# Kernel optimization log

Measured on AMD Instinct MI355X. Metric: run time of the kernel, lower is better.

Reference implementation:

```python
import jax, jax.numpy as jnp
import numpy as np

BN_EPS = 1e-5


def _binarize_act(x):
    # sign(x) forward, clipped STE backward (grad passes where |x|<1)
    xc = jnp.clip(x, -1.0, 1.0)
    return xc + jax.lax.stop_gradient(jnp.sign(x) - xc)


def _binarize_weight(w):
    # XNOR/ReActNet: per-out-channel scale * sign(w); clipped-STE gradient
    scale = jax.lax.stop_gradient(jnp.mean(jnp.abs(w), axis=(1, 2, 3), keepdims=True))
    wc = jnp.clip(w, -1.0, 1.0)
    return wc + jax.lax.stop_gradient(scale * jnp.sign(w) - wc)


def setup_inputs() -> dict:
    key = jax.random.key(0)
    ks = jax.random.split(key, 8)
    B, C, H, W = 64, 64, 56, 56
    P = 64  # planes == inplanes (stride 1, no downsample)
    x = jax.random.normal(ks[0], (B, C, H, W), dtype=jnp.float32)
    bias0 = jnp.zeros((1, C, 1, 1), dtype=jnp.float32)
    w = jax.random.normal(ks[1], (P, C, 3, 3), dtype=jnp.float32) * 0.1
    gamma = jnp.ones((P,), dtype=jnp.float32)
    beta = jnp.zeros((P,), dtype=jnp.float32)
    run_mean = jax.random.normal(ks[2], (P,), dtype=jnp.float32) * 0.1
    run_var = jax.random.uniform(ks[3], (P,), dtype=jnp.float32, minval=0.5, maxval=1.5)
    bias1 = jnp.zeros((1, P, 1, 1), dtype=jnp.float32)
    alpha = jnp.full((P,), 0.25, dtype=jnp.float32)  # PReLU default init
    bias2 = jnp.zeros((1, P, 1, 1), dtype=jnp.float32)
    return {"x": x, "bias0": bias0, "w": w, "gamma": gamma, "beta": beta,
            "run_mean": run_mean, "run_var": run_var, "bias1": bias1,
            "alpha": alpha, "bias2": bias2}


def reference(x, bias0, w, gamma, beta, run_mean, run_var, bias1, alpha, bias2):
    residual = x
    out = x + bias0                      # move0 (LearnableBias)
    out = _binarize_act(out)             # BinAct: sign, clipped STE
    bw = _binarize_weight(w)             # BinConv weight binarization
    out = jax.lax.conv_general_dilated(
        out, bw, window_strides=(1, 1), padding=((1, 1), (1, 1)),
        dimension_numbers=("NCHW", "OIHW", "NCHW"))
    # BatchNorm2d (inference form with running stats)
    inv = gamma / jnp.sqrt(run_var + BN_EPS)
    out = out * inv[None, :, None, None] + (beta - run_mean * inv)[None, :, None, None]
    out = out + residual                 # residual add (downsample is None)
    out = out + bias1                    # move1
    a = alpha[None, :, None, None]
    out = jnp.where(out >= 0, out, a * out)  # PReLU
    out = out + bias2                    # move2
    return out
```

## Files before the change

kernel.cpp:

```cpp
#include <hip/hip_runtime.h>

typedef unsigned long long u64;
typedef unsigned int u32;

#define BATCH 64
#define CH    64
#define HH    56
#define WW    56
#define HW    3136
#define NBAND 14
#define NBLK  (BATCH * NBAND)

__global__ __launch_bounds__(256)
void fold_kernel(const float* __restrict__ w,
                 const float* __restrict__ gamma,
                 const float* __restrict__ beta,
                 const float* __restrict__ rmean,
                 const float* __restrict__ rvar,
                 const float* __restrict__ bias1,
                 const float* __restrict__ alpha,
                 const float* __restrict__ bias2,
                 u64* __restrict__ wtab,
                 float* __restrict__ kc) {
    __shared__ float red[4];
    const int tid = threadIdx.x;
    const int lane = tid & 63;
    const int wv = tid >> 6;
    const int p = blockIdx.x;
    const float* wp = w + p * 576;

    float s = 0.f;
    for (int i = tid; i < 576; i += 256) s += fabsf(wp[i]);
#pragma unroll
    for (int off = 32; off > 0; off >>= 1) s += __shfl_down(s, off);
    if (lane == 0) red[wv] = s;
    __syncthreads();

    if (wv == 0) {
        u64 m[9];
#pragma unroll
        for (int t = 0; t < 9; ++t) {
            m[t] = __ballot(wp[lane * 9 + t] > 0.f);
            if (lane == 0) wtab[p * 12 + t] = m[t];
        }
        if (lane == 0) {
            float scale = (red[0] + red[1] + red[2] + red[3]) * (1.0f / 576.0f);
            float inv = gamma[p] * rsqrtf(rvar[p] + 1e-5f);
            float am = scale * inv;
            float bd = beta[p] - rmean[p] * inv + bias1[p];
            float pt[9];
#pragma unroll
            for (int t = 0; t < 9; ++t) pt[t] = (float)__popcll(m[t]);
            const float cL = pt[0] + pt[3] + pt[6];
            const float cR = pt[2] + pt[5] + pt[8];
            const float rT = pt[0] + pt[1] + pt[2];
            const float rB = pt[6] + pt[7] + pt[8];
            float Ci[3][3] = {
                {0.f, cL,                 cR},
                {rT,  rT + pt[3] + pt[6], rT + pt[5] + pt[8]},
                {rB,  rB + pt[0] + pt[3], rB + pt[2] + pt[5]}};
            float nv[3][3] = {{9, 6, 6}, {6, 4, 4}, {6, 4, 4}};
#pragma unroll
            for (int wc = 0; wc < 3; ++wc)
#pragma unroll
                for (int lc = 0; lc < 3; ++lc)
                    kc[(wc * 3 + lc) * 64 + p] =
                        fmaf(am, 64.f * nv[wc][lc] + 2.f * Ci[wc][lc], bd);
            float* cf = (float*)(wtab + p * 12 + 9);
            cf[0] = -2.f * am;
            cf[1] = alpha[p];
            cf[2] = bias2[p];
            cf[3] = 0.f;
            wtab[p * 12 + 11] = 0;
        }
    }
}

__global__ __launch_bounds__(512, 6)
void fused_kernel(const float* __restrict__ x,
                  const float* __restrict__ bias0,
                  const u64* __restrict__ wtab,
                  const float* __restrict__ kc,
                  float* __restrict__ out) {
    __shared__ __align__(16) u64 Lsgn[6][58];
    __shared__ __align__(16) float kcsm[576];

    const int tid = threadIdx.x;
    const int lane = tid & 63;
    const int wv = tid >> 6;

    for (int i = tid; i < 576; i += 512) kcsm[i] = kc[i];

    const int bid = blockIdx.x;
    const int wg = (bid & 7) * 112 + (bid >> 3);
    const int b = wg / NBAND;
    const int band = wg - b * NBAND;
    const int r0 = band * 4;

    if (wv < 6) {
        const int ir = r0 - 1 + wv;
        const bool rowok = (unsigned)ir < (unsigned)HH;
        u64 mine = 0;
        if (rowok) {
            const float* xp = x + ((size_t)(b * CH + lane)) * HW + ir * WW;
            const float bz = bias0[lane];
#pragma unroll
            for (int q = 0; q < 14; ++q) {
                float4 v = *(const float4*)(xp + q * 4);
                u64 m0 = __ballot(v.x + bz > 0.f);
                u64 m1 = __ballot(v.y + bz > 0.f);
                u64 m2 = __ballot(v.z + bz > 0.f);
                u64 m3 = __ballot(v.w + bz > 0.f);
                mine = (lane == q * 4 + 0) ? m0 : mine;
                mine = (lane == q * 4 + 1) ? m1 : mine;
                mine = (lane == q * 4 + 2) ? m2 : mine;
                mine = (lane == q * 4 + 3) ? m3 : mine;
            }
        }
        if (lane < WW)        Lsgn[wv][1 + lane] = mine;
        else if (lane == 56)  Lsgn[wv][0] = 0;
        else if (lane == 57)  Lsgn[wv][57] = 0;
    }
    __syncthreads();

    const int rl = wv & 3;
    const int ph = __builtin_amdgcn_readfirstlane((wv >> 2) << 5);
    const int h = r0 + rl;
    const int wl = min(lane, WW - 1);
    const bool active = lane < WW;

    u64 A0 = Lsgn[rl + 0][wl + 0];
    u64 A1 = Lsgn[rl + 0][wl + 1];
    u64 A2 = Lsgn[rl + 0][wl + 2];
    u64 A3 = Lsgn[rl + 1][wl + 0];
    u64 A4 = Lsgn[rl + 1][wl + 1];
    u64 A5 = Lsgn[rl + 1][wl + 2];
    u64 A6 = Lsgn[rl + 2][wl + 0];
    u64 A7 = Lsgn[rl + 2][wl + 1];
    u64 A8 = Lsgn[rl + 2][wl + 2];
    asm volatile("" : "+v"(A0), "+v"(A1), "+v"(A2), "+v"(A3), "+v"(A4),
                      "+v"(A5), "+v"(A6), "+v"(A7), "+v"(A8));

    const int wclass = (h == 0) ? 1 : (h == HH - 1) ? 2 : 0;
    const int lclass = (lane == 0) ? 1 : (lane == WW - 1) ? 2 : 0;
    const float* kp = kcsm + (wclass * 3 + lclass) * 64 + ph;

    const u32 base = (u32)(b * CH * HW + h * WW + wl) + (u32)ph * HW;

    float res[2][8];
#pragma unroll
    for (int j = 0; j < 8; ++j) res[0][j] = x[base + (u32)j * HW];
#pragma unroll
    for (int j = 0; j < 8; ++j) asm volatile("" : "+v"(res[0][j]));

#pragma unroll
    for (int c = 0; c < 4; ++c) {
        if (c < 3) {
#pragma unroll
            for (int j = 0; j < 8; ++j)
                res[(c + 1) & 1][j] = x[base + (u32)((c + 1) * 8 + j) * HW];
#pragma unroll
            for (int j = 0; j < 8; ++j)
                asm volatile("" : "+v"(res[(c + 1) & 1][j]));
        }
        float4 k0 = *(const float4*)(kp + c * 8);
        float4 k1 = *(const float4*)(kp + c * 8 + 4);
        float kv[8] = {k0.x, k0.y, k0.z, k0.w, k1.x, k1.y, k1.z, k1.w};

#pragma unroll
        for (int j = 0; j < 8; ++j) {
            const u64* wp = wtab + (ph + c * 8 + j) * 12;
            u32 P = 0;
            u64 v;
            v = A0 ^ wp[0]; P += __popc((u32)v); P += __popc((u32)(v >> 32));
            v = A1 ^ wp[1]; P += __popc((u32)v); P += __popc((u32)(v >> 32));
            v = A2 ^ wp[2]; P += __popc((u32)v); P += __popc((u32)(v >> 32));
            v = A3 ^ wp[3]; P += __popc((u32)v); P += __popc((u32)(v >> 32));
            v = A4 ^ wp[4]; P += __popc((u32)v); P += __popc((u32)(v >> 32));
            v = A5 ^ wp[5]; P += __popc((u32)v); P += __popc((u32)(v >> 32));
            v = A6 ^ wp[6]; P += __popc((u32)v); P += __popc((u32)(v >> 32));
            v = A7 ^ wp[7]; P += __popc((u32)v); P += __popc((u32)(v >> 32));
            v = A8 ^ wp[8]; P += __popc((u32)v); P += __popc((u32)(v >> 32));

            const float* cf = (const float*)(wp + 9);
            float o = fmaf(cf[0], (float)P, kv[j]) + res[c & 1][j];
            o = o >= 0.f ? o : cf[1] * o;
            o += cf[2];
            if (active) out[base + (u32)(c * 8 + j) * HW] = o;
        }
    }
}

extern "C" void kernel_launch(void* const* d_in, const int* in_sizes, int n_in,
                              void* d_out, int out_size, void* d_ws, size_t ws_size,
                              hipStream_t stream) {
    const float* x     = (const float*)d_in[0];
    const float* bias0 = (const float*)d_in[1];
    const float* w     = (const float*)d_in[2];
    const float* gamma = (const float*)d_in[3];
    const float* beta  = (const float*)d_in[4];
    const float* rmean = (const float*)d_in[5];
    const float* rvar  = (const float*)d_in[6];
    const float* bias1 = (const float*)d_in[7];
    const float* alpha = (const float*)d_in[8];
    const float* bias2 = (const float*)d_in[9];
    float* out = (float*)d_out;

    char* ws = (char*)d_ws;
    u64* wtab = (u64*)ws;
    float* kc = (float*)(ws + 6144);

    fold_kernel<<<64, 256, 0, stream>>>(
        w, gamma, beta, rmean, rvar, bias1, alpha, bias2, wtab, kc);

    fused_kernel<<<NBLK, 512, 0, stream>>>(x, bias0, wtab, kc, out);
}
```

Baseline: 52.44 us.

## Split sign packing into separate pass with padded global bitmask buffer

Sign-bit packing of the input moves out of the fused conv kernel into a prepass, which also absorbs weight folding. The prepass writes padded per-image bitmask rows to workspace. The conv kernel then reads its 3x3 neighbourhood straight from global memory, and each block handles one row with 256 threads covering 16 channels per wave. This removes the halo recomputation, in which each 4-row band re-read 6 rows of x, and the LDS sync. The cost is an extra global write and read of the packed bits and a second dependent launch.

```diff
diff --git a/kernel.cpp b/kernel.cpp
--- a/kernel.cpp
+++ b/kernel.cpp
@@ -8,11 +8,14 @@
 #define HH    56
 #define WW    56
 #define HW    3136
-#define NBAND 14
-#define NBLK  (BATCH * NBAND)
+#define SROW  64
+#define SIMG  (58 * SROW)
+#define PBLK  1792
 
 __global__ __launch_bounds__(256)
-void fold_kernel(const float* __restrict__ w,
+void pack_kernel(const float* __restrict__ x,
+                 const float* __restrict__ bias0,
+                 const float* __restrict__ w,
                  const float* __restrict__ gamma,
                  const float* __restrict__ beta,
                  const float* __restrict__ rmean,
@@ -20,124 +23,119 @@
                  const float* __restrict__ bias1,
                  const float* __restrict__ alpha,
                  const float* __restrict__ bias2,
+                 u64* __restrict__ Spk,
                  u64* __restrict__ wtab,
                  float* __restrict__ kc) {
-    __shared__ float red[4];
     const int tid = threadIdx.x;
     const int lane = tid & 63;
     const int wv = tid >> 6;
-    const int p = blockIdx.x;
-    const float* wp = w + p * 576;
-
-    float s = 0.f;
-    for (int i = tid; i < 576; i += 256) s += fabsf(wp[i]);
-#pragma unroll
-    for (int off = 32; off > 0; off >>= 1) s += __shfl_down(s, off);
-    if (lane == 0) red[wv] = s;
-    __syncthreads();
-
-    if (wv == 0) {
-        u64 m[9];
-#pragma unroll
-        for (int t = 0; t < 9; ++t) {
-            m[t] = __ballot(wp[lane * 9 + t] > 0.f);
-            if (lane == 0) wtab[p * 12 + t] = m[t];
-        }
-        if (lane == 0) {
-            float scale = (red[0] + red[1] + red[2] + red[3]) * (1.0f / 576.0f);
-            float inv = gamma[p] * rsqrtf(rvar[p] + 1e-5f);
-            float am = scale * inv;
-            float bd = beta[p] - rmean[p] * inv + bias1[p];
-            float pt[9];
-#pragma unroll
-            for (int t = 0; t < 9; ++t) pt[t] = (float)__popcll(m[t]);
-            const float cL = pt[0] + pt[3] + pt[6];
-            const float cR = pt[2] + pt[5] + pt[8];
-            const float rT = pt[0] + pt[1] + pt[2];
-            const float rB = pt[6] + pt[7] + pt[8];
-            float Ci[3][3] = {
-                {0.f, cL,                 cR},
-                {rT,  rT + pt[3] + pt[6], rT + pt[5] + pt[8]},
-                {rB,  rB + pt[0] + pt[3], rB + pt[2] + pt[5]}};
-            float nv[3][3] = {{9, 6, 6}, {6, 4, 4}, {6, 4, 4}};
-#pragma unroll
-            for (int wc = 0; wc < 3; ++wc)
-#pragma unroll
-                for (int lc = 0; lc < 3; ++lc)
-                    kc[(wc * 3 + lc) * 64 + p] =
-                        fmaf(am, 64.f * nv[wc][lc] + 2.f * Ci[wc][lc], bd);
-            float* cf = (float*)(wtab + p * 12 + 9);
-            cf[0] = -2.f * am;
-            cf[1] = alpha[p];
-            cf[2] = bias2[p];
-            cf[3] = 0.f;
-            wtab[p * 12 + 11] = 0;
+    const int blk = blockIdx.x;
+
+    if (blk < PBLK) {
+        const int half = blk & 1;
+        const int w0 = half * 28;
+        const int row = (blk >> 1) * 4 + wv;
+        const int b = row / HH;
+        const int h = row - b * HH;
+        const float* xp = x + ((size_t)(b * CH + lane)) * HW + h * WW + w0;
+        const float bz = bias0[lane];
+        u64 mine = 0;
+#pragma unroll
+        for (int q = 0; q < 7; ++q) {
+            float4 v = *(const float4*)(xp + q * 4);
+            u64 m0 = __ballot(v.x + bz > 0.f);
+            u64 m1 = __ballot(v.y + bz > 0.f);
+            u64 m2 = __ballot(v.z + bz > 0.f);
+            u64 m3 = __ballot(v.w + bz > 0.f);
+            mine = (lane == q * 4 + 0) ? m0 : mine;
+            mine = (lane == q * 4 + 1) ? m1 : mine;
+            mine = (lane == q * 4 + 2) ? m2 : mine;
+            mine = (lane == q * 4 + 3) ? m3 : mine;
+        }
+        u64* sp = Spk + (size_t)b * SIMG + (h + 1) * SROW;
+        if (lane < 28) sp[1 + w0 + lane] = mine;
+        if (half == 0 && lane == 28) sp[0] = 0;
+        if (half == 1 && lane == 28) sp[57] = 0;
+        if (h == 0 && lane >= 29 && lane < 58)
+            Spk[(size_t)b * SIMG + half * 29 + (lane - 29)] = 0;
+        if (h == HH - 1 && lane >= 29 && lane < 58)
+            Spk[(size_t)b * SIMG + 57 * SROW + half * 29 + (lane - 29)] = 0;
+    } else {
+        __shared__ float red[4];
+        const int p = blk - PBLK;
+        const float* wp = w + p * 576;
+        float s = 0.f;
+        for (int i = tid; i < 576; i += 256) s += fabsf(wp[i]);
+#pragma unroll
+        for (int off = 32; off > 0; off >>= 1) s += __shfl_down(s, off);
+        if (lane == 0) red[wv] = s;
+        __syncthreads();
+
+        if (wv == 0) {
+            u64 m[9];
+#pragma unroll
+            for (int t = 0; t < 9; ++t) {
+                m[t] = __ballot(wp[lane * 9 + t] > 0.f);
+                if (lane == 0) wtab[p * 12 + t] = m[t];
+            }
+            if (lane == 0) {
+                float scale = (red[0] + red[1] + red[2] + red[3]) * (1.0f / 576.0f);
+                float inv = gamma[p] * rsqrtf(rvar[p] + 1e-5f);
+                float am = scale * inv;
+                float bd = beta[p] - rmean[p] * inv + bias1[p];
+                float pt[9];
+#pragma unroll
+                for (int t = 0; t < 9; ++t) pt[t] = (float)__popcll(m[t]);
+                const float cL = pt[0] + pt[3] + pt[6];
+                const float cR = pt[2] + pt[5] + pt[8];
+                const float rT = pt[0] + pt[1] + pt[2];
+                const float rB = pt[6] + pt[7] + pt[8];
+                float Ci[3][3] = {
+                    {0.f, cL,                 cR},
+                    {rT,  rT + pt[3] + pt[6], rT + pt[5] + pt[8]},
+                    {rB,  rB + pt[0] + pt[3], rB + pt[2] + pt[5]}};
+                float nv[3][3] = {{9, 6, 6}, {6, 4, 4}, {6, 4, 4}};
+#pragma unroll
+                for (int wc = 0; wc < 3; ++wc)
+#pragma unroll
+                    for (int lc = 0; lc < 3; ++lc)
+                        kc[(wc * 3 + lc) * 64 + p] =
+                            fmaf(am, 64.f * nv[wc][lc] + 2.f * Ci[wc][lc], bd);
+                float* cf = (float*)(wtab + p * 12 + 9);
+                cf[0] = -2.f * am;
+                cf[1] = alpha[p];
+                cf[2] = bias2[p];
+                cf[3] = 0.f;
+                wtab[p * 12 + 11] = 0;
+            }
         }
     }
 }
 
-__global__ __launch_bounds__(512, 6)
-void fused_kernel(const float* __restrict__ x,
-                  const float* __restrict__ bias0,
-                  const u64* __restrict__ wtab,
-                  const float* __restrict__ kc,
-                  float* __restrict__ out) {
-    __shared__ __align__(16) u64 Lsgn[6][58];
+__global__ __launch_bounds__(256, 8)
+void conv_kernel(const u64* __restrict__ Spk,
+                 const u64* __restrict__ wtab,
+                 const float* __restrict__ kc,
+                 const float* __restrict__ x,
+                 float* __restrict__ out) {
     __shared__ __align__(16) float kcsm[576];
-
     const int tid = threadIdx.x;
+    for (int i = tid; i < 576; i += 256) kcsm[i] = kc[i];
+    __syncthreads();
+
+    const int bid = blockIdx.x;
+    const int wg = (bid & 7) * 448 + (bid >> 3);
     const int lane = tid & 63;
-    const int wv = tid >> 6;
-
-    for (int i = tid; i < 576; i += 512) kcsm[i] = kc[i];
-
-    const int bid = blockIdx.x;
-    const int wg = (bid & 7) * 112 + (bid >> 3);
-    const int b = wg / NBAND;
-    const int band = wg - b * NBAND;
-    const int r0 = band * 4;
-
-    if (wv < 6) {
-        const int ir = r0 - 1 + wv;
-        const bool rowok = (unsigned)ir < (unsigned)HH;
-        u64 mine = 0;
-        if (rowok) {
-            const float* xp = x + ((size_t)(b * CH + lane)) * HW + ir * WW;
-            const float bz = bias0[lane];
-#pragma unroll
-            for (int q = 0; q < 14; ++q) {
-                float4 v = *(const float4*)(xp + q * 4);
-                u64 m0 = __ballot(v.x + bz > 0.f);
-                u64 m1 = __ballot(v.y + bz > 0.f);
-                u64 m2 = __ballot(v.z + bz > 0.f);
-                u64 m3 = __ballot(v.w + bz > 0.f);
-                mine = (lane == q * 4 + 0) ? m0 : mine;
-                mine = (lane == q * 4 + 1) ? m1 : mine;
-                mine = (lane == q * 4 + 2) ? m2 : mine;
-                mine = (lane == q * 4 + 3) ? m3 : mine;
-            }
-        }
-        if (lane < WW)        Lsgn[wv][1 + lane] = mine;
-        else if (lane == 56)  Lsgn[wv][0] = 0;
-        else if (lane == 57)  Lsgn[wv][57] = 0;
-    }
-    __syncthreads();
-
-    const int rl = wv & 3;
-    const int ph = __builtin_amdgcn_readfirstlane((wv >> 2) << 5);
-    const int h = r0 + rl;
+    const int ph = __builtin_amdgcn_readfirstlane((tid >> 6) << 4);
+    const int b = wg / HH;
+    const int h = wg - b * HH;
     const int wl = min(lane, WW - 1);
     const bool active = lane < WW;
 
-    u64 A0 = Lsgn[rl + 0][wl + 0];
-    u64 A1 = Lsgn[rl + 0][wl + 1];
-    u64 A2 = Lsgn[rl + 0][wl + 2];
-    u64 A3 = Lsgn[rl + 1][wl + 0];
-    u64 A4 = Lsgn[rl + 1][wl + 1];
-    u64 A5 = Lsgn[rl + 1][wl + 2];
-    u64 A6 = Lsgn[rl + 2][wl + 0];
-    u64 A7 = Lsgn[rl + 2][wl + 1];
-    u64 A8 = Lsgn[rl + 2][wl + 2];
+    const u64* ap = Spk + (size_t)b * SIMG + (h + 1) * SROW + (wl + 1);
+    u64 A0 = ap[-SROW - 1], A1 = ap[-SROW], A2 = ap[-SROW + 1];
+    u64 A3 = ap[-1],        A4 = ap[0],     A5 = ap[1];
+    u64 A6 = ap[SROW - 1],  A7 = ap[SROW],  A8 = ap[SROW + 1];
     asm volatile("" : "+v"(A0), "+v"(A1), "+v"(A2), "+v"(A3), "+v"(A4),
                       "+v"(A5), "+v"(A6), "+v"(A7), "+v"(A8));
 
@@ -154,14 +152,13 @@
     for (int j = 0; j < 8; ++j) asm volatile("" : "+v"(res[0][j]));
 
 #pragma unroll
-    for (int c = 0; c < 4; ++c) {
-        if (c < 3) {
+    for (int c = 0; c < 2; ++c) {
+        if (c < 1) {
 #pragma unroll
             for (int j = 0; j < 8; ++j)
-                res[(c + 1) & 1][j] = x[base + (u32)((c + 1) * 8 + j) * HW];
-#pragma unroll
-            for (int j = 0; j < 8; ++j)
-                asm volatile("" : "+v"(res[(c + 1) & 1][j]));
+                res[1][j] = x[base + (u32)(8 + j) * HW];
+#pragma unroll
+            for (int j = 0; j < 8; ++j) asm volatile("" : "+v"(res[1][j]));
         }
         float4 k0 = *(const float4*)(kp + c * 8);
         float4 k1 = *(const float4*)(kp + c * 8 + 4);
@@ -183,7 +180,7 @@
             v = A8 ^ wp[8]; P += __popc((u32)v); P += __popc((u32)(v >> 32));
 
             const float* cf = (const float*)(wp + 9);
-            float o = fmaf(cf[0], (float)P, kv[j]) + res[c & 1][j];
+            float o = fmaf(cf[0], (float)P, kv[j]) + res[c][j];
             o = o >= 0.f ? o : cf[1] * o;
             o += cf[2];
             if (active) out[base + (u32)(c * 8 + j) * HW] = o;
@@ -209,9 +206,11 @@
     char* ws = (char*)d_ws;
     u64* wtab = (u64*)ws;
     float* kc = (float*)(ws + 6144);
-
-    fold_kernel<<<64, 256, 0, stream>>>(
-        w, gamma, beta, rmean, rvar, bias1, alpha, bias2, wtab, kc);
-
-    fused_kernel<<<NBLK, 512, 0, stream>>>(x, bias0, wtab, kc, out);
+    u64* Spk  = (u64*)(ws + 16384);
+
+    pack_kernel<<<PBLK + 64, 256, 0, stream>>>(
+        x, bias0, w, gamma, beta, rmean, rvar, bias1, alpha, bias2,
+        Spk, wtab, kc);
+
+    conv_kernel<<<BATCH * HH, 256, 0, stream>>>(Spk, wtab, kc, x, out);
 }
```

After: 56.67 us. +8.1%, slower.
